# Kernel optimization log

Measured on AMD Instinct MI355X. Metric: run time of the kernel, lower is better.

Reference implementation:

```python
import jax, jax.numpy as jnp
import numpy as np
import math

B, S, D, H, L, DFF, NHEADS_OUT = 2, 1024, 1024, 16, 4, 4096, 3
DK = D // H
LN_EPS = 1e-5


def setup_inputs() -> dict:
    key = jax.random.key(0)
    ks = jax.random.split(key, 16)
    w = lambda k, shp: jax.random.normal(k, shp, dtype=jnp.float32) * 0.02
    return {
        "src": jax.random.normal(ks[0], (B, S, 1), dtype=jnp.float32),
        "emb_w": w(ks[1], (1, D)), "emb_b": jnp.zeros((D,), jnp.float32),
        "pe": w(ks[2], (S, D)),
        "Wq": w(ks[3], (L, D, D)), "bq": jnp.zeros((L, D), jnp.float32),
        "Wk": w(ks[4], (L, D, D)), "bk": jnp.zeros((L, D), jnp.float32),
        "Wv": w(ks[5], (L, D, D)), "bv": jnp.zeros((L, D), jnp.float32),
        "Wo": w(ks[6], (L, D, D)), "bo": jnp.zeros((L, D), jnp.float32),
        "fc1_w": w(ks[7], (L, D, DFF)), "fc1_b": jnp.zeros((L, DFF), jnp.float32),
        "fc2_w": w(ks[8], (L, DFF, D)), "fc2_b": jnp.zeros((L, D), jnp.float32),
        "ln1_g": jnp.ones((L, D), jnp.float32), "ln1_b": jnp.zeros((L, D), jnp.float32),
        "ln2_g": jnp.ones((L, D), jnp.float32), "ln2_b": jnp.zeros((L, D), jnp.float32),
        "hw1": w(ks[9], (NHEADS_OUT, D, D)), "hb1": jnp.zeros((NHEADS_OUT, D), jnp.float32),
        "hw2": w(ks[10], (NHEADS_OUT, D, 1)), "hb2": jnp.zeros((NHEADS_OUT, 1), jnp.float32),
    }


def _layernorm(x, g, b):
    mu = jnp.mean(x, axis=-1, keepdims=True)
    var = jnp.mean((x - mu) ** 2, axis=-1, keepdims=True)
    return (x - mu) * jax.lax.rsqrt(var + LN_EPS) * g + b


def _custom_softmax(x):
    # faithful to module's custom_softmax: max (inf->0), exp, sum + 1e-9
    m = jnp.max(x, axis=-1, keepdims=True)
    m = jnp.where(jnp.isinf(m), 0.0, m)
    e = jnp.exp(x - m)
    return e / (jnp.sum(e, axis=-1, keepdims=True) + 1e-9)


def _attention(x, Wq, bq, Wk, bk, Wv, bv, Wo, bo, mask):
    b, s, d = x.shape
    split = lambda t: t.reshape(b, s, H, DK).transpose(0, 2, 1, 3)  # [B,H,S,DK]
    q = split(x @ Wq + bq)
    k = split(x @ Wk + bk)
    v = split(x @ Wv + bv)
    scores = jnp.einsum('bhqd,bhkd->bhqk', q, k) / math.sqrt(DK)
    scores = jnp.where(mask, scores, -jnp.inf)
    probs = _custom_softmax(scores)
    out = jnp.einsum('bhqk,bhkd->bhqd', probs, v)
    out = out.transpose(0, 2, 1, 3).reshape(b, s, d)
    return out @ Wo + bo


def reference(src, emb_w, emb_b, pe, Wq, bq, Wk, bk, Wv, bv, Wo, bo,
              fc1_w, fc1_b, fc2_w, fc2_b, ln1_g, ln1_b, ln2_g, ln2_b,
              hw1, hb1, hw2, hb2):
    s = src.shape[1]
    mask = jnp.tril(jnp.ones((s, s), dtype=bool))[None, None]  # causal [1,1,S,S]
    x = src @ emb_w + emb_b          # [B,S,D]
    x = x + pe[:s]                   # learned positional encoding
    for l in range(L):
        attn = _attention(x, Wq[l], bq[l], Wk[l], bk[l], Wv[l], bv[l], Wo[l], bo[l], mask)
        h = _layernorm(x + attn, ln1_g[l], ln1_b[l])
        x = h + attn                 # quirk in original forward_step
        ff = jax.nn.relu(jax.nn.relu(x @ fc1_w[l] + fc1_b[l]) @ fc2_w[l] + fc2_b[l])
        h2 = _layernorm(x + ff, ln2_g[l], ln2_b[l])
        x = h2 + ff                  # quirk in original forward_step
    # output_size independent 2-layer heads, each -> scalar; stack on last dim
    hid = jax.nn.relu(jnp.einsum('bsd,odf->bsof', x, hw1) + hb1[None, None])  # [B,S,3,D]
    out = jnp.einsum('bsof,ofe->bsoe', hid, hw2) + hb2[None, None]            # [B,S,3,1]
    return out[..., 0]               # [B,S,3]
```

## Files before the change

### kernel.cpp

```cpp
#include <hip/hip_runtime.h>
#include <hip/hip_bf16.h>


#define BB 2
#define SS 1024
#define DD 1024
#define HH 16
#define LL 4
#define DFFC 4096
#define DKC 64

typedef __attribute__((ext_vector_type(8))) short short8;
typedef __attribute__((ext_vector_type(4))) float f32x4;

#define GLD16(gptr, ldsptr) \
    __builtin_amdgcn_global_load_lds( \
        (const __attribute__((address_space(1))) unsigned int*)(gptr), \
        (__attribute__((address_space(3))) unsigned int*)(ldsptr), 16, 0, 0)

__device__ __forceinline__ float ldin(const void* p, long long i, int isbf) {
    if (isbf) {
        unsigned int u = ((unsigned int)((const unsigned short*)p)[i]) << 16;
        return __uint_as_float(u);
    }
    return ((const float*)p)[i];
}
__device__ __forceinline__ unsigned short f2bf(float f) {
    unsigned int u = __float_as_uint(f);
    return (unsigned short)((u + 0x7FFFu + ((u >> 16) & 1u)) >> 16);
}
__device__ __forceinline__ float bf2f(unsigned short h) {
    return __uint_as_float(((unsigned int)h) << 16);
}
__device__ __forceinline__ void atomAddF(float* p, float v) {
    __hip_atomic_fetch_add(p, v, __ATOMIC_RELAXED, __HIP_MEMORY_SCOPE_AGENT);
}

__global__ void k_detect(const void* __restrict__ ln1g, int* __restrict__ flag) {
    unsigned int w = *(const unsigned int*)ln1g;
    *flag = (w == 0x3F800000u) ? 0 : 1;
}

__global__ __launch_bounds__(256) void k_zero(float4* __restrict__ p) {
    p[(size_t)blockIdx.x * 256 + threadIdx.x] = make_float4(0.f, 0.f, 0.f, 0.f);
}

__global__ void k_embed(const void* __restrict__ src, const void* __restrict__ emb_w,
                        const void* __restrict__ emb_b, const void* __restrict__ pe,
                        float* __restrict__ x, unsigned short* __restrict__ xb,
                        const int* __restrict__ flag) {
    int row = blockIdx.x;
    int s = row & (SS - 1);
    int isbf = *flag;
    float sv = ldin(src, row, isbf);
    for (int d = threadIdx.x; d < DD; d += 256) {
        float v = sv * ldin(emb_w, d, isbf) + ldin(emb_b, d, isbf) + ldin(pe, (long long)s * DD + d, isbf);
        x[(long long)row * DD + d] = v;
        xb[(long long)row * DD + d] = f2bf(v);
    }
}

struct TSlot { const void* src; long long off; int ldw; int nrows; int ncols; long long dstoff; };
struct TArgs { TSlot s[4]; };

__global__ __launch_bounds__(256) void k_wtrans(TArgs ta, unsigned short* __restrict__ dst,
                                                const int* __restrict__ flag) {
    TSlot sl = ta.s[blockIdx.z];
    if (!sl.src) return;
    int k0 = blockIdx.x * 64, n0 = blockIdx.y * 64;
    if (k0 >= sl.nrows || n0 >= sl.ncols) return;
    int isbf = *flag;
    __shared__ float tile[64][65];
    int tid = threadIdx.x;
    int c = tid & 63, rg = tid >> 6;
    #pragma unroll
    for (int i = 0; i < 16; i++) {
        int kr = rg * 16 + i;
        tile[kr][c] = ldin(sl.src, sl.off + (long long)(k0 + kr) * sl.ldw + n0 + c, isbf);
    }
    __syncthreads();
    int nr = tid >> 2, kc = (tid & 3) * 16;
    unsigned short* dp = dst + sl.dstoff + (long long)(n0 + nr) * sl.nrows + k0 + kc;
    unsigned short h[16];
    #pragma unroll
    for (int j = 0; j < 16; j++) h[j] = f2bf(tile[kc + j][nr]);
    uint4 u0, u1;
    u0.x = h[0] | (h[1] << 16);  u0.y = h[2] | (h[3] << 16);
    u0.z = h[4] | (h[5] << 16);  u0.w = h[6] | (h[7] << 16);
    u1.x = h[8] | (h[9] << 16);  u1.y = h[10] | (h[11] << 16);
    u1.z = h[12] | (h[13] << 16); u1.w = h[14] | (h[15] << 16);
    *(uint4*)&dp[0] = u0;
    *(uint4*)&dp[8] = u1;
}

struct BiasArgs { const void* p[4]; long long o[4]; };

template <int MF, int NF>
__global__ __launch_bounds__(256) void k_gemm_mfma(
    const unsigned short* __restrict__ A, int lda,
    const unsigned short* __restrict__ Wt, int ktot,
    int ksplit, BiasArgs ba,
    float* __restrict__ C, int ldc, int atomicC,
    unsigned short* __restrict__ Cb, int ldcb,
    int act, const int* __restrict__ flag)
{
    const int BM = 32 * MF;
    const int BN = 32 * NF;
    __shared__ __align__(16) unsigned short As[2][BM * 32];
    __shared__ __align__(16) unsigned short Bs[2][BN * 32];
    int bflag = *flag;
    int tid = threadIdx.x;
    int wave = tid >> 6, lane = tid & 63, quad = lane >> 4, l16 = lane & 15;
    int wm = (wave & 1) * 16 * MF, wn = (wave >> 1) * 16 * NF;
    int bm = blockIdx.y * BM, bn = blockIdx.x * BN;
    int kb = blockIdx.z * ksplit;
    int srow = lane >> 2;
    int scol = (lane & 3) * 8;

    f32x4 acc[MF][NF];
    #pragma unroll
    for (int i = 0; i < MF; i++)
        #pragma unroll
        for (int j = 0; j < NF; j++) acc[i][j] = (f32x4){0.f, 0.f, 0.f, 0.f};

    const unsigned short* Abase = A + (size_t)bm * lda + kb;

    auto stage = [&](int k0, int p) {
        #pragma unroll
        for (int i = 0; i < MF / 2; i++) {
            int s = wave * (MF / 2) + i;
            GLD16(Abase + (size_t)(s * 16 + srow) * lda + k0 + scol, &As[p][(s * 16) * 32]);
        }
        #pragma unroll
        for (int i = 0; i < NF / 2; i++) {
            int s = wave * (NF / 2) + i;
            GLD16(Wt + (size_t)(bn + s * 16 + srow) * ktot + kb + k0 + scol, &Bs[p][(s * 16) * 32]);
        }
    };

    int nk = ksplit >> 5;
    stage(0, 0);
    for (int it = 0; it < nk; it++) {
        int p = it & 1;
        __syncthreads();
        if (it + 1 < nk) stage((it + 1) << 5, p ^ 1);

        short8 af[MF], bf[NF];
        #pragma unroll
        for (int mi = 0; mi < MF; mi++)
            af[mi] = *(const short8*)&As[p][(wm + mi * 16 + l16) * 32 + quad * 8];
        #pragma unroll
        for (int ni = 0; ni < NF; ni++)
            bf[ni] = *(const short8*)&Bs[p][(wn + ni * 16 + l16) * 32 + quad * 8];
        #pragma unroll
        for (int mi = 0; mi < MF; mi++)
            #pragma unroll
            for (int ni = 0; ni < NF; ni++)
                acc[mi][ni] = __builtin_amdgcn_mfma_f32_16x16x32_bf16(af[mi], bf[ni], acc[mi][ni], 0, 0, 0);
    }

    #pragma unroll
    for (int ni = 0; ni < NF; ni++) {
        int cn = bn + wn + ni * 16 + l16;
        float bval = 0.0f;
        if (ba.p[0]) {
            int sel = cn >> 10;
            bval = ldin(ba.p[sel], ba.o[sel] + (cn & 1023), bflag);
        }
        #pragma unroll
        for (int mi = 0; mi < MF; mi++) {
            #pragma unroll
            for (int rr = 0; rr < 4; rr++) {
                int cm = bm + wm + mi * 16 + quad * 4 + rr;
                float v = acc[mi][ni][rr] + bval;
                if (act) v = fmaxf(v, 0.0f);
                if (atomicC) {
                    atomAddF(&C[(size_t)cm * ldc + cn], v);
                } else {
                    if (C) C[(size_t)cm * ldc + cn] = v;
                    if (Cb) Cb[(size_t)cm * ldcb + cn] = f2bf(v);
                }
            }
        }
    }
}

__global__ __launch_bounds__(256) void k_attn(const unsigned short* __restrict__ qkv,
                                              float* __restrict__ part0,
                                              float* __restrict__ part1,
                                              float* __restrict__ rs)
{
    __shared__ __align__(16) unsigned short Vt[2][64 * 72];
    __shared__ __align__(16) unsigned short Ps[4][16 * 72];

    int tid = threadIdx.x;
    int wave = tid >> 6, lane = tid & 63, quad = lane >> 4, l16 = lane & 15;

    int flat = blockIdx.x + (blockIdx.y << 4) + (blockIdx.z << 9);
    int xcd = flat & 7;
    int j = flat >> 3;
    int bh = ((j >> 5) << 3) + xcd;
    int r = j & 31;
    int split = r >> 4;
    int qt = 15 - (r & 15);

    int b = bh >> 4, h = bh & 15;
    int q0 = qt * 64;
    int qbase = q0 + wave * 16;

    int nk = qt + 1;
    int half = (nk + 1) >> 1;
    int kt0 = split ? half : 0;
    int kt1 = split ? nk : half;

    const unsigned short* qrow = qkv + (size_t)(b * SS + qbase + l16) * 3072 + h * DKC;
    short8 aq0 = *(const short8*)(qrow + quad * 8);
    short8 aq1 = *(const short8*)(qrow + 32 + quad * 8);

    f32x4 oacc[4];
    #pragma unroll
    for (int nt = 0; nt < 4; nt++) oacc[nt] = (f32x4){0.f, 0.f, 0.f, 0.f};
    float rsum[4] = {0.f, 0.f, 0.f, 0.f};

    int kp = tid & 31;
    int vc = (tid >> 5) * 8;
    unsigned short* pw = &Ps[wave][0];

    short8 vs0, vs1;
    auto loadV = [&](int k0) {
        const unsigned short* v0 = qkv + (size_t)(b * SS + k0 + 2 * kp) * 3072 + 2048 + h * DKC + vc;
        vs0 = *(const short8*)v0;
        vs1 = *(const short8*)(v0 + 3072);
    };
    auto writeV = [&](int p) {
        unsigned int* vt32 = (unsigned int*)&Vt[p][0];
        #pragma unroll
        for (int i = 0; i < 8; i++) {
            unsigned int pr = ((unsigned int)(unsigned short)vs0[i]) |
                              (((unsigned int)(unsigned short)vs1[i]) << 16);
            vt32[(vc + i) * 36 + kp] = pr;
        }
    };

    short8 kc0[4], kc1[4];
    auto loadK = [&](int k0, short8 (&d0)[4], short8 (&d1)[4]) {
        #pragma unroll
        for (int nt = 0; nt < 4; nt++) {
            const unsigned short* krow =
                qkv + (size_t)(b * SS + k0 + nt * 16 + l16) * 3072 + 1024 + h * DKC + quad * 8;
            d0[nt] = *(const short8*)(krow);
            d1[nt] = *(const short8*)(krow + 32);
        }
    };

    if (kt0 < kt1) {
        loadV(kt0 * 64);
        loadK(kt0 * 64, kc0, kc1);
        writeV(0);
    }
    for (int kt = kt0; kt < kt1; kt++) {
        int k0 = kt * 64;
        int p = (kt - kt0) & 1;
        __syncthreads();

        short8 kn0[4], kn1[4];
        int havenext = (kt + 1 < kt1);
        if (havenext) {
            loadV(k0 + 64);
            loadK(k0 + 64, kn0, kn1);
        }

        f32x4 sacc[4];
        #pragma unroll
        for (int nt = 0; nt < 4; nt++) {
            sacc[nt] = (f32x4){0.f, 0.f, 0.f, 0.f};
            sacc[nt] = __builtin_amdgcn_mfma_f32_16x16x32_bf16(aq0, kc0[nt], sacc[nt], 0, 0, 0);
            sacc[nt] = __builtin_amdgcn_mfma_f32_16x16x32_bf16(aq1, kc1[nt], sacc[nt], 0, 0, 0);
        }

        #pragma unroll
        for (int nt = 0; nt < 4; nt++) {
            int key = k0 + nt * 16 + l16;
            #pragma unroll
            for (int rr = 0; rr < 4; rr++) {
                float pv = __expf(sacc[nt][rr] * 0.125f);
                if (key > qbase + quad * 4 + rr) pv = 0.0f;
                rsum[rr] += pv;
                pw[(quad * 4 + rr) * 72 + nt * 16 + l16] = f2bf(pv);
            }
        }

        short8 ap0 = *(const short8*)&pw[l16 * 72 + quad * 8];
        short8 ap1 = *(const short8*)&pw[l16 * 72 + 32 + quad * 8];
        #pragma unroll
        for (int nt = 0; nt < 4; nt++) {
            short8 bv0 = *(const short8*)&Vt[p][(nt * 16 + l16) * 72 + quad * 8];
            short8 bv1 = *(const short8*)&Vt[p][(nt * 16 + l16) * 72 + 32 + quad * 8];
            oacc[nt] = __builtin_amdgcn_mfma_f32_16x16x32_bf16(ap0, bv0, oacc[nt], 0, 0, 0);
            oacc[nt] = __builtin_amdgcn_mfma_f32_16x16x32_bf16(ap1, bv1, oacc[nt], 0, 0, 0);
        }

        if (havenext) {
            writeV(p ^ 1);
            #pragma unroll
            for (int nt = 0; nt < 4; nt++) { kc0[nt] = kn0[nt]; kc1[nt] = kn1[nt]; }
        }
    }

    #pragma unroll
    for (int m = 1; m < 16; m <<= 1) {
        #pragma unroll
        for (int rr = 0; rr < 4; rr++)
            rsum[rr] += __shfl_xor(rsum[rr], m, 64);
    }
    float* part = split ? part1 : part0;
    #pragma unroll
    for (int rr = 0; rr < 4; rr++) {
        int q = qbase + quad * 4 + rr;
        size_t obase = (size_t)(b * SS + q) * 1024 + h * DKC;
        #pragma unroll
        for (int nt = 0; nt < 4; nt++)
            part[obase + nt * 16 + l16] = oacc[nt][rr];
        if (l16 == 0)
            rs[(((size_t)split * 2 + b) * 16 + h) * 1024 + q] = rsum[rr];
    }
}

__global__ __launch_bounds__(256) void k_comb(const float* __restrict__ p0,
                                              const float* __restrict__ p1,
                                              const float* __restrict__ rs,
                                              unsigned short* __restrict__ qkv)
{
    int row = blockIdx.x;
    int b = row >> 10, q = row & 1023;
    int tid = threadIdx.x;
    int col = tid * 4;
    int h = col >> 6;
    float r0 = rs[(((size_t)0 + b) * 16 + h) * 1024 + q];
    float r1 = rs[(((size_t)2 + b) * 16 + h) * 1024 + q];
    float inv = 1.0f / (r0 + r1 + 1e-9f);
    size_t base = (size_t)row * 1024 + col;
    float4 a = *(const float4*)(p0 + base);
    float4 c = *(const float4*)(p1 + base);
    unsigned short* dst = qkv + (size_t)row * 3072 + col;
    uint2 w;
    w.x = f2bf((a.x + c.x) * inv) | (f2bf((a.y + c.y) * inv) << 16);
    w.y = f2bf((a.z + c.z) * inv) | (f2bf((a.w + c.w) * inv) << 16);
    *(uint2*)dst = w;
}

__global__ __launch_bounds__(256) void k_addlnadd(float* __restrict__ x, const float* __restrict__ t,
                                                  const void* __restrict__ tbias, long long tboff, int tact,
                                                  const void* __restrict__ g, long long goff,
                                                  const void* __restrict__ bta, long long boff,
                                                  unsigned short* __restrict__ xb,
                                                  const int* __restrict__ flag)
{
    int row = blockIdx.x;
    int tid = threadIdx.x;
    int isbf = *flag;
    __shared__ float red[256];
    long long base = (long long)row * DD;

    float yv[4], tv[4];
    float lsum = 0.0f;
    #pragma unroll
    for (int i = 0; i < 4; i++) {
        int d = tid + i * 256;
        float tt = t[base + d] + ldin(tbias, tboff + d, isbf);
        if (tact) tt = fmaxf(tt, 0.0f);
        tv[i] = tt;
        yv[i] = x[base + d] + tt;
        lsum += yv[i];
    }
    red[tid] = lsum;
    __syncthreads();
    for (int s = 128; s > 0; s >>= 1) {
        if (tid < s) red[tid] += red[tid + s];
        __syncthreads();
    }
    float mu = red[0] * (1.0f / DD);
    __syncthreads();

    float lv = 0.0f;
    #pragma unroll
    for (int i = 0; i < 4; i++) {
        float dl = yv[i] - mu;
        lv += dl * dl;
    }
    red[tid] = lv;
    __syncthreads();
    for (int s = 128; s > 0; s >>= 1) {
        if (tid < s) red[tid] += red[tid + s];
        __syncthreads();
    }
    float rsq = rsqrtf(red[0] * (1.0f / DD) + 1e-5f);

    #pragma unroll
    for (int i = 0; i < 4; i++) {
        int d = tid + i * 256;
        float nrm = (yv[i] - mu) * rsq * ldin(g, goff + d, isbf) + ldin(bta, boff + d, isbf);
        float xo = nrm + tv[i];
        x[base + d] = xo;
        xb[base + d] = f2bf(xo);
    }
}

__global__ __launch_bounds__(256) void k_head(const unsigned short* __restrict__ hid,
                                              const void* __restrict__ hw2,
                                              const void* __restrict__ hb2,
                                              void* __restrict__ out,
                                              const int* __restrict__ flag)
{
    int row = blockIdx.x;
    int o = blockIdx.y;
    int tid = threadIdx.x;
    int isbf = *flag;
    __shared__ float red[256];
    long long base = (long long)row * 3072 + o * 1024;
    float acc = 0.0f;
    for (int f = tid; f < DD; f += 256)
        acc += bf2f(hid[base + f]) * ldin(hw2, (long long)o * DD + f, isbf);
    red[tid] = acc;
    __syncthreads();
    for (int s = 128; s > 0; s >>= 1) {
        if (tid < s) red[tid] += red[tid + s];
        __syncthreads();
    }
    if (tid == 0) {
        float r = red[0] + ldin(hb2, o, isbf);
        long long idx = (long long)row * 3 + o;
        if (isbf) ((__hip_bfloat16*)out)[idx] = __float2bfloat16(r);
        else      ((float*)out)[idx] = r;
    }
}

extern "C" void kernel_launch(void* const* d_in, const int* in_sizes, int n_in,
                              void* d_out, int out_size, void* d_ws, size_t ws_size,
                              hipStream_t stream) {
    char* w = (char*)d_ws;
    int* flag = (int*)w;
    const size_t NA = (size_t)BB * SS * DD;
    float* x  = (float*)(w + 256);
    float* tb = x + NA;
    unsigned short* qkv = (unsigned short*)(tb + NA);
    unsigned short* hb  = qkv + (size_t)BB * SS * 3072;
    unsigned short* wbuf = hb + (size_t)BB * SS * 2048;
    unsigned short* xb = wbuf + 4 * (size_t)DD * DD;
    float* rsbuf = (float*)(xb + NA);
    unsigned short* f1 = qkv;

    const long long MM = (long long)DD * DD;
    dim3 blk(256);
    TSlot z = {nullptr, 0, 1, 0, 0, 0};
    BiasArgs nb = {{nullptr, nullptr, nullptr, nullptr}, {0, 0, 0, 0}};

    k_detect<<<1, 1, 0, stream>>>(d_in[16], flag);
    k_embed<<<BB * SS, blk, 0, stream>>>(d_in[0], d_in[1], d_in[2], d_in[3], x, xb, flag);

    for (int l = 0; l < LL; l++) {
        long long wo = (long long)l * MM;
        long long bo = (long long)l * DD;
        {
            TArgs ta = {{ {d_in[4],  wo, DD, DD, DD, 0},
                          {d_in[6],  wo, DD, DD, DD, MM},
                          {d_in[8],  wo, DD, DD, DD, 2 * MM},
                          {d_in[10], wo, DD, DD, DD, 3 * MM} }};
            k_wtrans<<<dim3(16, 16, 4), blk, 0, stream>>>(ta, wbuf, flag);
        }
        {
            BiasArgs qb = {{d_in[5], d_in[7], d_in[9], nullptr}, {bo, bo, bo, 0}};
            k_gemm_mfma<2, 4><<<dim3(24, 32), blk, 0, stream>>>(
                xb, DD, wbuf, DD, DD, qb, nullptr, 0, 0, qkv, 3072, 0, flag);
        }
        k_attn<<<dim3(16, BB * HH, 2), blk, 0, stream>>>(qkv, tb, (float*)hb, rsbuf);
        k_comb<<<BB * SS, blk, 0, stream>>>(tb, (float*)hb, rsbuf, qkv);
        k_zero<<<2048, blk, 0, stream>>>((float4*)tb);
        k_gemm_mfma<2, 4><<<dim3(8, 32, 4), blk, 0, stream>>>(
            qkv, 3072, wbuf + 3 * MM, DD, 256, nb, tb, DD, 1, nullptr, 0, 0, flag);
        k_addlnadd<<<BB * SS, blk, 0, stream>>>(x, tb, d_in[11], bo, 0,
                                                d_in[16], bo, d_in[17], bo, xb, flag);
        {
            TArgs ta = {{ {d_in[12], (long long)l * DD * DFFC, DFFC, DD, DFFC, 0}, z, z, z }};
            k_wtrans<<<dim3(16, 64, 1), blk, 0, stream>>>(ta, wbuf, flag);
        }
        {
            long long f1b0 = (long long)l * DFFC;
            BiasArgs fb = {{d_in[13], d_in[13], d_in[13], d_in[13]},
                           {f1b0, f1b0 + 1024, f1b0 + 2048, f1b0 + 3072}};
            k_gemm_mfma<2, 4><<<dim3(32, 32), blk, 0, stream>>>(
                xb, DD, wbuf, DD, DD, fb, nullptr, 0, 0, f1, DFFC, 1, flag);
        }
        {
            TArgs ta = {{ {d_in[14], (long long)l * DFFC * DD, DD, DFFC, DD, 0}, z, z, z }};
            k_wtrans<<<dim3(64, 16, 1), blk, 0, stream>>>(ta, wbuf, flag);
        }
        k_zero<<<2048, blk, 0, stream>>>((float4*)tb);
        k_gemm_mfma<2, 4><<<dim3(8, 32, 4), blk, 0, stream>>>(
            f1, DFFC, wbuf, DFFC, 1024, nb, tb, DD, 1, nullptr, 0, 0, flag);
        k_addlnadd<<<BB * SS, blk, 0, stream>>>(x, tb, d_in[15], bo, 1,
                                                d_in[18], bo, d_in[19], bo, xb, flag);
    }

    {
        TArgs ta = {{ {d_in[20], 0 * MM, DD, DD, DD, 0},
                      {d_in[20], 1 * MM, DD, DD, DD, MM},
                      {d_in[20], 2 * MM, DD, DD, DD, 2 * MM}, z }};
        k_wtrans<<<dim3(16, 16, 3), blk, 0, stream>>>(ta, wbuf, flag);
    }
    {
        BiasArgs hbias = {{d_in[21], d_in[21], d_in[21], nullptr}, {0, 1024, 2048, 0}};
        k_gemm_mfma<2, 4><<<dim3(24, 32), blk, 0, stream>>>(
            xb, DD, wbuf, DD, DD, hbias, nullptr, 0, 0, qkv, 3072, 1, flag);
    }
    k_head<<<dim3(BB * SS, 3), blk, 0, stream>>>(qkv, d_in[22], d_in[23], d_out, flag);
}
```

Before: 1.219 ms.

## Replace atomic split-K reductions with two partial buffers and chunked FFN

Split-K GEMMs now write to two separate fp32 partial buffers, one per z-slice, instead of zeroing a buffer and atomically adding four slices. The add+layernorm kernel sums the two partials, which removes the zero kernels and the atomic traffic. The FFN is processed in two 2048-wide chunks that accumulate into the partials with read-modify-write, and fc1/fc2 weight transposes are merged into one launch per chunk. The LDS staging layout is also changed to a fragment-contiguous order so each lane reads 16 contiguous bytes. The cost is more GEMM launches for the FFN and an extra read of the partials.

```diff
diff --git a/kernel.cpp b/kernel.cpp
--- a/kernel.cpp
+++ b/kernel.cpp
@@ -32,17 +32,10 @@
 __device__ __forceinline__ float bf2f(unsigned short h) {
     return __uint_as_float(((unsigned int)h) << 16);
 }
-__device__ __forceinline__ void atomAddF(float* p, float v) {
-    __hip_atomic_fetch_add(p, v, __ATOMIC_RELAXED, __HIP_MEMORY_SCOPE_AGENT);
-}
 
 __global__ void k_detect(const void* __restrict__ ln1g, int* __restrict__ flag) {
     unsigned int w = *(const unsigned int*)ln1g;
     *flag = (w == 0x3F800000u) ? 0 : 1;
-}
-
-__global__ __launch_bounds__(256) void k_zero(float4* __restrict__ p) {
-    p[(size_t)blockIdx.x * 256 + threadIdx.x] = make_float4(0.f, 0.f, 0.f, 0.f);
 }
 
 __global__ void k_embed(const void* __restrict__ src, const void* __restrict__ emb_w,
@@ -100,12 +93,14 @@
     const unsigned short* __restrict__ A, int lda,
     const unsigned short* __restrict__ Wt, int ktot,
     int ksplit, BiasArgs ba,
-    float* __restrict__ C, int ldc, int atomicC,
+    float* __restrict__ C0, float* __restrict__ C1, int ldc, int accum,
     unsigned short* __restrict__ Cb, int ldcb,
     int act, const int* __restrict__ flag)
 {
     const int BM = 32 * MF;
     const int BN = 32 * NF;
+    const int AU = (BM / 16) / 4;
+    const int BU = (BN / 16) / 4;
     __shared__ __align__(16) unsigned short As[2][BM * 32];
     __shared__ __align__(16) unsigned short Bs[2][BN * 32];
     int bflag = *flag;
@@ -114,8 +109,9 @@
     int wm = (wave & 1) * 16 * MF, wn = (wave >> 1) * 16 * NF;
     int bm = blockIdx.y * BM, bn = blockIdx.x * BN;
     int kb = blockIdx.z * ksplit;
-    int srow = lane >> 2;
-    int scol = (lane & 3) * 8;
+    int srow = lane & 15;
+    int scol = (lane >> 4) * 8;
+    float* Cz = (blockIdx.z == 0) ? C0 : C1;
 
     f32x4 acc[MF][NF];
     #pragma unroll
@@ -127,14 +123,14 @@
 
     auto stage = [&](int k0, int p) {
         #pragma unroll
-        for (int i = 0; i < MF / 2; i++) {
-            int s = wave * (MF / 2) + i;
-            GLD16(Abase + (size_t)(s * 16 + srow) * lda + k0 + scol, &As[p][(s * 16) * 32]);
-        }
-        #pragma unroll
-        for (int i = 0; i < NF / 2; i++) {
-            int s = wave * (NF / 2) + i;
-            GLD16(Wt + (size_t)(bn + s * 16 + srow) * ktot + kb + k0 + scol, &Bs[p][(s * 16) * 32]);
+        for (int i = 0; i < AU; i++) {
+            int rs = wave * AU + i;
+            GLD16(Abase + (size_t)(rs * 16 + srow) * lda + k0 + scol, &As[p][rs * 512]);
+        }
+        #pragma unroll
+        for (int i = 0; i < BU; i++) {
+            int rs = wave * BU + i;
+            GLD16(Wt + (size_t)(bn + rs * 16 + srow) * ktot + kb + k0 + scol, &Bs[p][rs * 512]);
         }
     };
 
@@ -148,10 +144,10 @@
         short8 af[MF], bf[NF];
         #pragma unroll
         for (int mi = 0; mi < MF; mi++)
-            af[mi] = *(const short8*)&As[p][(wm + mi * 16 + l16) * 32 + quad * 8];
+            af[mi] = *(const short8*)&As[p][((wave & 1) * MF + mi) * 512 + lane * 8];
         #pragma unroll
         for (int ni = 0; ni < NF; ni++)
-            bf[ni] = *(const short8*)&Bs[p][(wn + ni * 16 + l16) * 32 + quad * 8];
+            bf[ni] = *(const short8*)&Bs[p][((wave >> 1) * NF + ni) * 512 + lane * 8];
         #pragma unroll
         for (int mi = 0; mi < MF; mi++)
             #pragma unroll
@@ -172,14 +168,12 @@
             #pragma unroll
             for (int rr = 0; rr < 4; rr++) {
                 int cm = bm + wm + mi * 16 + quad * 4 + rr;
+                size_t idx = (size_t)cm * ldc + cn;
                 float v = acc[mi][ni][rr] + bval;
+                if (accum && Cz) v += Cz[idx];
                 if (act) v = fmaxf(v, 0.0f);
-                if (atomicC) {
-                    atomAddF(&C[(size_t)cm * ldc + cn], v);
-                } else {
-                    if (C) C[(size_t)cm * ldc + cn] = v;
-                    if (Cb) Cb[(size_t)cm * ldcb + cn] = f2bf(v);
-                }
+                if (Cz) Cz[idx] = v;
+                if (Cb) Cb[(size_t)cm * ldcb + cn] = f2bf(v);
             }
         }
     }
@@ -349,7 +343,9 @@
     *(uint2*)dst = w;
 }
 
-__global__ __launch_bounds__(256) void k_addlnadd(float* __restrict__ x, const float* __restrict__ t,
+__global__ __launch_bounds__(256) void k_addlnadd(float* __restrict__ x,
+                                                  const float* __restrict__ t0,
+                                                  const float* __restrict__ t1,
                                                   const void* __restrict__ tbias, long long tboff, int tact,
                                                   const void* __restrict__ g, long long goff,
                                                   const void* __restrict__ bta, long long boff,
@@ -367,7 +363,7 @@
     #pragma unroll
     for (int i = 0; i < 4; i++) {
         int d = tid + i * 256;
-        float tt = t[base + d] + ldin(tbias, tboff + d, isbf);
+        float tt = t0[base + d] + (t1 ? t1[base + d] : 0.0f) + ldin(tbias, tboff + d, isbf);
         if (tact) tt = fmaxf(tt, 0.0f);
         tv[i] = tt;
         yv[i] = x[base + d] + tt;
@@ -448,7 +444,9 @@
     unsigned short* wbuf = hb + (size_t)BB * SS * 2048;
     unsigned short* xb = wbuf + 4 * (size_t)DD * DD;
     float* rsbuf = (float*)(xb + NA);
-    unsigned short* f1 = qkv;
+    float* P0 = tb;
+    float* P1 = (float*)hb;
+    unsigned short* f1h = qkv;
 
     const long long MM = (long long)DD * DD;
     dim3 blk(256);
@@ -471,34 +469,34 @@
         {
             BiasArgs qb = {{d_in[5], d_in[7], d_in[9], nullptr}, {bo, bo, bo, 0}};
             k_gemm_mfma<2, 4><<<dim3(24, 32), blk, 0, stream>>>(
-                xb, DD, wbuf, DD, DD, qb, nullptr, 0, 0, qkv, 3072, 0, flag);
-        }
-        k_attn<<<dim3(16, BB * HH, 2), blk, 0, stream>>>(qkv, tb, (float*)hb, rsbuf);
-        k_comb<<<BB * SS, blk, 0, stream>>>(tb, (float*)hb, rsbuf, qkv);
-        k_zero<<<2048, blk, 0, stream>>>((float4*)tb);
-        k_gemm_mfma<2, 4><<<dim3(8, 32, 4), blk, 0, stream>>>(
-            qkv, 3072, wbuf + 3 * MM, DD, 256, nb, tb, DD, 1, nullptr, 0, 0, flag);
-        k_addlnadd<<<BB * SS, blk, 0, stream>>>(x, tb, d_in[11], bo, 0,
+                xb, DD, wbuf, DD, DD, qb, nullptr, nullptr, 0, 0, qkv, 3072, 0, flag);
+        }
+        k_attn<<<dim3(16, BB * HH, 2), blk, 0, stream>>>(qkv, P0, P1, rsbuf);
+        k_comb<<<BB * SS, blk, 0, stream>>>(P0, P1, rsbuf, qkv);
+        k_gemm_mfma<2, 4><<<dim3(8, 32, 2), blk, 0, stream>>>(
+            qkv, 3072, wbuf + 3 * MM, DD, 512, nb, P0, P1, DD, 0, nullptr, 0, 0, flag);
+        k_addlnadd<<<BB * SS, blk, 0, stream>>>(x, P0, P1, d_in[11], bo, 0,
                                                 d_in[16], bo, d_in[17], bo, xb, flag);
-        {
-            TArgs ta = {{ {d_in[12], (long long)l * DD * DFFC, DFFC, DD, DFFC, 0}, z, z, z }};
-            k_wtrans<<<dim3(16, 64, 1), blk, 0, stream>>>(ta, wbuf, flag);
-        }
-        {
-            long long f1b0 = (long long)l * DFFC;
-            BiasArgs fb = {{d_in[13], d_in[13], d_in[13], d_in[13]},
-                           {f1b0, f1b0 + 1024, f1b0 + 2048, f1b0 + 3072}};
-            k_gemm_mfma<2, 4><<<dim3(32, 32), blk, 0, stream>>>(
-                xb, DD, wbuf, DD, DD, fb, nullptr, 0, 0, f1, DFFC, 1, flag);
-        }
-        {
-            TArgs ta = {{ {d_in[14], (long long)l * DFFC * DD, DD, DFFC, DD, 0}, z, z, z }};
-            k_wtrans<<<dim3(64, 16, 1), blk, 0, stream>>>(ta, wbuf, flag);
-        }
-        k_zero<<<2048, blk, 0, stream>>>((float4*)tb);
-        k_gemm_mfma<2, 4><<<dim3(8, 32, 4), blk, 0, stream>>>(
-            f1, DFFC, wbuf, DFFC, 1024, nb, tb, DD, 1, nullptr, 0, 0, flag);
-        k_addlnadd<<<BB * SS, blk, 0, stream>>>(x, tb, d_in[15], bo, 1,
+        for (int c = 0; c < 2; c++) {
+            long long w1off = (long long)l * DD * DFFC + (long long)c * 2048;
+            long long f1b0 = (long long)l * DFFC + (long long)c * 2048;
+            long long w2off = (long long)l * DFFC * DD + (long long)c * 2048 * DD;
+            {
+                TArgs ta = {{ {d_in[12], w1off, DFFC, DD, 2048, 0},
+                              {d_in[14], w2off, DD, 2048, DD, 2 * MM}, z, z }};
+                k_wtrans<<<dim3(32, 32, 2), blk, 0, stream>>>(ta, wbuf, flag);
+            }
+            {
+                BiasArgs fb = {{d_in[13], d_in[13], nullptr, nullptr},
+                               {f1b0, f1b0 + 1024, 0, 0}};
+                k_gemm_mfma<2, 4><<<dim3(16, 32), blk, 0, stream>>>(
+                    xb, DD, wbuf, DD, DD, fb, nullptr, nullptr, 0, 0, f1h, 2048, 1, flag);
+            }
+            k_gemm_mfma<2, 4><<<dim3(8, 32, 2), blk, 0, stream>>>(
+                f1h, 2048, wbuf + 2 * MM, 2048, 1024, nb, P0, P1, DD, c,
+                nullptr, 0, 0, flag);
+        }
+        k_addlnadd<<<BB * SS, blk, 0, stream>>>(x, P0, P1, d_in[15], bo, 1,
                                                 d_in[18], bo, d_in[19], bo, xb, flag);
     }
 
@@ -511,7 +509,7 @@
     {
         BiasArgs hbias = {{d_in[21], d_in[21], d_in[21], nullptr}, {0, 1024, 2048, 0}};
         k_gemm_mfma<2, 4><<<dim3(24, 32), blk, 0, stream>>>(
-            xb, DD, wbuf, DD, DD, hbias, nullptr, 0, 0, qkv, 3072, 1, flag);
+            xb, DD, wbuf, DD, DD, hbias, nullptr, nullptr, 0, 0, qkv, 3072, 1, flag);
     }
     k_head<<<dim3(BB * SS, 3), blk, 0, stream>>>(qkv, d_in[22], d_in[23], d_out, flag);
 }
```

After: 1.389 ms. 13.9% more time.
